# Optimization experiments

Hardware: AMD Instinct MI355X
Metric: run time of the kernel (lower is better)

## Reference

```python
import jax, jax.numpy as jnp
import numpy as np

N = 16384
E = 65536

def _nnconv(x, src, dst, edge_attr, A, b, root, bias, c_in, c_out):
    # edge MLP: [E,2] -> [E, c_in*c_out], ReLU
    W = jax.nn.relu(edge_attr @ A + b).reshape(E, c_in, c_out)
    # gather source features, per-edge matmul: [E,c_in] x [E,c_in,c_out] -> [E,c_out]
    msg = jnp.einsum('ei,eio->eo', x[src], W)
    # scatter-add to target nodes
    agg = jax.ops.segment_sum(msg, dst, num_segments=N)
    return agg + x @ root + bias

def setup_inputs() -> dict:
    key = jax.random.key(0)
    ks = jax.random.split(key, 12)
    inp = {
        'x': jax.random.normal(ks[0], (N, 8), dtype=jnp.float32),
        'edge_index': jax.random.randint(ks[1], (2, E), 0, N, dtype=jnp.int64),
        'edge_attr': jax.random.normal(ks[2], (E, 2), dtype=jnp.float32),
        # edge-MLP 1: Linear(2, 512)
        'A1': jax.random.normal(ks[3], (2, 512), dtype=jnp.float32) * (1.0 / np.sqrt(2.0)),
        'b1': jnp.zeros((512,), dtype=jnp.float32),
        # edge-MLP 2: Linear(2, 4096)
        'A2': jax.random.normal(ks[4], (2, 4096), dtype=jnp.float32) * (1.0 / np.sqrt(2.0)),
        'b2': jnp.zeros((4096,), dtype=jnp.float32),
        # NNConv root weights + biases
        'root1': jax.random.normal(ks[5], (8, 64), dtype=jnp.float32) * (1.0 / np.sqrt(8.0)),
        'bias1': jnp.zeros((64,), dtype=jnp.float32),
        'root2': jax.random.normal(ks[6], (64, 64), dtype=jnp.float32) * (1.0 / np.sqrt(64.0)),
        'bias2': jnp.zeros((64,), dtype=jnp.float32),
    }
    return inp

def reference(x, edge_index, edge_attr, A1, b1, A2, b2, root1, bias1, root2, bias2):
    src = edge_index[0]  # x_j (message source)
    dst = edge_index[1]  # aggregation target
    h = _nnconv(x, src, dst, edge_attr, A1, b1, root1, bias1, 8, 64)
    h = _nnconv(h, src, dst, edge_attr, A2, b2, root2, bias2, 64, 64)
    return h
```

## Files before the change

kernel.cpp:

```cpp
#include <hip/hip_runtime.h>

#define N_NODES 16384
#define N_EDGES 65536

typedef float f32x16 __attribute__((ext_vector_type(16)));
typedef float f32x8  __attribute__((ext_vector_type(8)));
typedef float f32x4  __attribute__((ext_vector_type(4)));

__device__ __forceinline__ float rfl_f(float v) {
    int i = __builtin_amdgcn_readfirstlane(__builtin_bit_cast(int, v));
    return __builtin_bit_cast(float, i);
}

__global__ void k_node1(const float* __restrict__ x, const float* __restrict__ root1,
                        const float* __restrict__ bias1, float* __restrict__ h1) {
    int t = blockIdx.x * blockDim.x + threadIdx.x;
    int n = t >> 6, o = t & 63;
    float acc = bias1[o];
#pragma unroll
    for (int i = 0; i < 8; ++i)
        acc = fmaf(x[n * 8 + i], root1[i * 64 + o], acc);
    h1[t] = acc;
}

__global__ __launch_bounds__(256)
void k_edge1(const float* __restrict__ x, const int* __restrict__ ei,
             const float* __restrict__ ea, const float* __restrict__ A1,
             const float* __restrict__ b1, float* __restrict__ h1) {
    int lane = threadIdx.x & 63;
    f32x8 W0, W1, BB;
#pragma unroll
    for (int i = 0; i < 8; ++i) {
        W0[i] = A1[i * 64 + lane];
        W1[i] = A1[512 + i * 64 + lane];
        BB[i] = b1[i * 64 + lane];
    }
    asm volatile("" : "+v"(W0), "+v"(W1), "+v"(BB));

    int wid = blockIdx.x * (blockDim.x >> 6) + (threadIdx.x >> 6);
    int nw = gridDim.x * (blockDim.x >> 6);
#pragma clang loop unroll(disable)
    for (int p = wid; p < N_EDGES / 2; p += nw) {
        int2 srcp = ((const int2*)ei)[p];
        int2 dstp = ((const int2*)(ei + N_EDGES))[p];
        float4 eap = ((const float4*)ea)[p];
        int s0 = __builtin_amdgcn_readfirstlane(srcp.x);
        int s1 = __builtin_amdgcn_readfirstlane(srcp.y);
        int d0 = __builtin_amdgcn_readfirstlane(dstp.x);
        int d1 = __builtin_amdgcn_readfirstlane(dstp.y);
        float ea00 = rfl_f(eap.x), ea01 = rfl_f(eap.y);
        float ea10 = rfl_f(eap.z), ea11 = rfl_f(eap.w);
        const float* xp0 = x + (size_t)s0 * 8;
        const float* xp1 = x + (size_t)s1 * 8;
        f32x8 ha, hb;
        asm volatile("s_load_dwordx8 %0, %2, 0x0\n\t"
                     "s_load_dwordx8 %1, %3, 0x0\n\t"
                     "s_waitcnt lgkmcnt(0)"
                     : "=&s"(ha), "=&s"(hb) : "s"(xp0), "s"(xp1));
        float acc0 = 0.f, acc1 = 0.f;
#pragma unroll
        for (int i = 0; i < 8; ++i) {
            float wva = fmaxf(fmaf(ea01, W1[i], fmaf(ea00, W0[i], BB[i])), 0.f);
            acc0 = fmaf(ha[i], wva, acc0);
            float wvb = fmaxf(fmaf(ea11, W1[i], fmaf(ea10, W0[i], BB[i])), 0.f);
            acc1 = fmaf(hb[i], wvb, acc1);
        }
        atomicAdd(&h1[(size_t)d0 * 64 + lane], acc0);
        atomicAdd(&h1[(size_t)d1 * 64 + lane], acc1);
    }
}

__global__ __launch_bounds__(256)
void k_node2(const float* __restrict__ h1, const float* __restrict__ root2,
             const float* __restrict__ bias2, float* __restrict__ out) {
    int lane = threadIdx.x & 63;
    f32x16 R0, R1, R2, R3;
#pragma unroll
    for (int i = 0; i < 16; ++i) {
        R0[i] = root2[(i)      * 64 + lane];
        R1[i] = root2[(16 + i) * 64 + lane];
        R2[i] = root2[(32 + i) * 64 + lane];
        R3[i] = root2[(48 + i) * 64 + lane];
    }
    asm volatile("" : "+v"(R0), "+v"(R1), "+v"(R2), "+v"(R3));
    float bias = bias2[lane];

    int wid = blockIdx.x * (blockDim.x >> 6) + (threadIdx.x >> 6);
    int nw = gridDim.x * (blockDim.x >> 6);
#pragma clang loop unroll(disable)
    for (int n = wid; n < N_NODES; n += nw) {
        int nu = __builtin_amdgcn_readfirstlane(n);
        const float* hp = h1 + (size_t)nu * 64;
        f32x16 h0, h1v, h2, h3;
        asm volatile("s_load_dwordx16 %0, %4, 0x0\n\t"
                     "s_load_dwordx16 %1, %4, 0x40\n\t"
                     "s_load_dwordx16 %2, %4, 0x80\n\t"
                     "s_load_dwordx16 %3, %4, 0xc0\n\t"
                     "s_waitcnt lgkmcnt(0)"
                     : "=&s"(h0), "=&s"(h1v), "=&s"(h2), "=&s"(h3) : "s"(hp));
        float acc = bias;
#pragma unroll
        for (int i = 0; i < 16; ++i) acc = fmaf(h0[i],  R0[i], acc);
#pragma unroll
        for (int i = 0; i < 16; ++i) acc = fmaf(h1v[i], R1[i], acc);
#pragma unroll
        for (int i = 0; i < 16; ++i) acc = fmaf(h2[i],  R2[i], acc);
#pragma unroll
        for (int i = 0; i < 16; ++i) acc = fmaf(h3[i],  R3[i], acc);
        out[(size_t)nu * 64 + lane] = acc;
    }
}

__global__ __launch_bounds__(256)
void k_edge2(const float* __restrict__ h1, const int* __restrict__ ei,
             const float* __restrict__ ea, const float* __restrict__ A2,
             const float* __restrict__ b2, float* __restrict__ out) {
    __shared__ __align__(16) float WT[3 * 64 * 36];
    int half = blockIdx.x & 1;
    for (int j = threadIdx.x; j < 2048; j += 256) {
        int i = j >> 6, o = j & 63;
        WT[o * 36 + i]                = A2[half * 2048 + j];
        WT[64 * 36 + o * 36 + i]      = A2[4096 + half * 2048 + j];
        WT[2 * 64 * 36 + o * 36 + i]  = b2[half * 2048 + j];
    }
    __syncthreads();

    int lane = threadIdx.x & 63;
    int base = half * 32;
    unsigned laddr = (unsigned)(uintptr_t)WT + lane * 144;

    int g = blockIdx.x >> 1;
    int wslot = g * 4 + (threadIdx.x >> 6);
#pragma clang loop unroll(disable)
    for (int p = wslot; p < N_EDGES / 2; p += 4096) {
        int2 srcp = ((const int2*)ei)[p];
        int2 dstp = ((const int2*)(ei + N_EDGES))[p];
        float4 eap = ((const float4*)ea)[p];
        int s0 = __builtin_amdgcn_readfirstlane(srcp.x);
        int s1 = __builtin_amdgcn_readfirstlane(srcp.y);
        int d0 = __builtin_amdgcn_readfirstlane(dstp.x);
        int d1 = __builtin_amdgcn_readfirstlane(dstp.y);
        float ea00 = rfl_f(eap.x), ea01 = rfl_f(eap.y);
        float ea10 = rfl_f(eap.z), ea11 = rfl_f(eap.w);
        const float* hp0 = h1 + (size_t)s0 * 64 + base;
        const float* hp1 = h1 + (size_t)s1 * 64 + base;

        f32x16 ha, hb, hc, hd;
        asm volatile("s_load_dwordx16 %0, %4, 0x0\n\t"
                     "s_load_dwordx16 %1, %4, 0x40\n\t"
                     "s_load_dwordx16 %2, %5, 0x0\n\t"
                     "s_load_dwordx16 %3, %5, 0x40"
                     : "=&s"(ha), "=&s"(hb), "=&s"(hc), "=&s"(hd)
                     : "s"(hp0), "s"(hp1));

        f32x4 wa[8], wb[8], wc[8];
        asm volatile(
            "ds_read_b128 %0, %12 offset:0\n\t"
            "ds_read_b128 %1, %12 offset:16\n\t"
            "ds_read_b128 %2, %12 offset:32\n\t"
            "ds_read_b128 %3, %12 offset:48\n\t"
            "ds_read_b128 %4, %12 offset:9216\n\t"
            "ds_read_b128 %5, %12 offset:9232\n\t"
            "ds_read_b128 %6, %12 offset:9248\n\t"
            "ds_read_b128 %7, %12 offset:9264\n\t"
            "ds_read_b128 %8, %12 offset:18432\n\t"
            "ds_read_b128 %9, %12 offset:18448\n\t"
            "ds_read_b128 %10, %12 offset:18464\n\t"
            "ds_read_b128 %11, %12 offset:18480"
            : "=&v"(wa[0]), "=&v"(wa[1]), "=&v"(wa[2]), "=&v"(wa[3]),
              "=&v"(wb[0]), "=&v"(wb[1]), "=&v"(wb[2]), "=&v"(wb[3]),
              "=&v"(wc[0]), "=&v"(wc[1]), "=&v"(wc[2]), "=&v"(wc[3])
            : "v"(laddr));
        asm volatile(
            "ds_read_b128 %0, %12 offset:64\n\t"
            "ds_read_b128 %1, %12 offset:80\n\t"
            "ds_read_b128 %2, %12 offset:96\n\t"
            "ds_read_b128 %3, %12 offset:112\n\t"
            "ds_read_b128 %4, %12 offset:9280\n\t"
            "ds_read_b128 %5, %12 offset:9296\n\t"
            "ds_read_b128 %6, %12 offset:9312\n\t"
            "ds_read_b128 %7, %12 offset:9328\n\t"
            "ds_read_b128 %8, %12 offset:18496\n\t"
            "ds_read_b128 %9, %12 offset:18512\n\t"
            "ds_read_b128 %10, %12 offset:18528\n\t"
            "ds_read_b128 %11, %12 offset:18544"
            : "=&v"(wa[4]), "=&v"(wa[5]), "=&v"(wa[6]), "=&v"(wa[7]),
              "=&v"(wb[4]), "=&v"(wb[5]), "=&v"(wb[6]), "=&v"(wb[7]),
              "=&v"(wc[4]), "=&v"(wc[5]), "=&v"(wc[6]), "=&v"(wc[7])
            : "v"(laddr));
        asm volatile("s_waitcnt lgkmcnt(0)"
            : "+v"(wa[0]), "+v"(wa[1]), "+v"(wa[2]), "+v"(wa[3]),
              "+v"(wa[4]), "+v"(wa[5]), "+v"(wa[6]), "+v"(wa[7]),
              "+v"(wb[0]), "+v"(wb[1]), "+v"(wb[2]), "+v"(wb[3]),
              "+v"(wb[4]), "+v"(wb[5]), "+v"(wb[6]), "+v"(wb[7]),
              "+v"(wc[0]), "+v"(wc[1]), "+v"(wc[2]), "+v"(wc[3]),
              "+v"(wc[4]), "+v"(wc[5]), "+v"(wc[6]), "+v"(wc[7]),
              "+s"(ha), "+s"(hb), "+s"(hc), "+s"(hd));

        float acc0 = 0.f, acc1 = 0.f;
#pragma unroll
        for (int q = 0; q < 4; ++q) {
#pragma unroll
            for (int k = 0; k < 4; ++k) {
                float wv0 = fmaxf(fmaf(ea01, wb[q][k], fmaf(ea00, wa[q][k], wc[q][k])), 0.f);
                acc0 = fmaf(ha[q * 4 + k], wv0, acc0);
                float wv1 = fmaxf(fmaf(ea11, wb[q][k], fmaf(ea10, wa[q][k], wc[q][k])), 0.f);
                acc1 = fmaf(hc[q * 4 + k], wv1, acc1);
            }
        }
#pragma unroll
        for (int q = 4; q < 8; ++q) {
#pragma unroll
            for (int k = 0; k < 4; ++k) {
                float wv0 = fmaxf(fmaf(ea01, wb[q][k], fmaf(ea00, wa[q][k], wc[q][k])), 0.f);
                acc0 = fmaf(hb[(q - 4) * 4 + k], wv0, acc0);
                float wv1 = fmaxf(fmaf(ea11, wb[q][k], fmaf(ea10, wa[q][k], wc[q][k])), 0.f);
                acc1 = fmaf(hd[(q - 4) * 4 + k], wv1, acc1);
            }
        }
        atomicAdd(&out[(size_t)d0 * 64 + lane], acc0);
        atomicAdd(&out[(size_t)d1 * 64 + lane], acc1);
    }
}

extern "C" void kernel_launch(void* const* d_in, const int* in_sizes, int n_in,
                              void* d_out, int out_size, void* d_ws, size_t ws_size,
                              hipStream_t stream) {
    const float* x     = (const float*)d_in[0];
    const int*   ei    = (const int*)d_in[1];
    const float* ea    = (const float*)d_in[2];
    const float* A1    = (const float*)d_in[3];
    const float* b1    = (const float*)d_in[4];
    const float* A2    = (const float*)d_in[5];
    const float* b2    = (const float*)d_in[6];
    const float* root1 = (const float*)d_in[7];
    const float* bias1 = (const float*)d_in[8];
    const float* root2 = (const float*)d_in[9];
    const float* bias2 = (const float*)d_in[10];
    float* out = (float*)d_out;
    float* h1  = (float*)d_ws;

    k_node1<<<N_NODES * 64 / 256, 256, 0, stream>>>(x, root1, bias1, h1);
    k_edge1<<<2048, 256, 0, stream>>>(x, ei, ea, A1, b1, h1);
    k_node2<<<1024, 256, 0, stream>>>(h1, root2, bias2, out);
    k_edge2<<<2048, 256, 0, stream>>>(h1, ei, ea, A2, b2, out);
}
```

Baseline: 144.3 us.

## Software-pipeline edge2 loop by prefetching next source rows and edge data

Restructures the layer-2 edge loop so that the scalar loads of the next iteration's source-node feature rows are issued partway through the current iteration's FMA work. Edge indices and attributes are fetched two iterations ahead. This aims to hide the latency of the dependent scalar-memory gather behind compute. The risk is that the inline-asm s_load results are written asynchronously into SGPRs the compiler believes are already defined, and that pressure on scalar and vector registers goes up.

```diff
diff --git a/kernel.cpp b/kernel.cpp
--- a/kernel.cpp
+++ b/kernel.cpp
@@ -119,40 +119,44 @@
     int half = blockIdx.x & 1;
     for (int j = threadIdx.x; j < 2048; j += 256) {
         int i = j >> 6, o = j & 63;
-        WT[o * 36 + i]                = A2[half * 2048 + j];
-        WT[64 * 36 + o * 36 + i]      = A2[4096 + half * 2048 + j];
-        WT[2 * 64 * 36 + o * 36 + i]  = b2[half * 2048 + j];
+        WT[o * 36 + i]               = A2[half * 2048 + j];
+        WT[64 * 36 + o * 36 + i]     = A2[4096 + half * 2048 + j];
+        WT[2 * 64 * 36 + o * 36 + i] = b2[half * 2048 + j];
     }
     __syncthreads();
 
     int lane = threadIdx.x & 63;
-    int base = half * 32;
+    int base = __builtin_amdgcn_readfirstlane(half * 32);
     unsigned laddr = (unsigned)(uintptr_t)WT + lane * 144;
 
     int g = blockIdx.x >> 1;
     int wslot = g * 4 + (threadIdx.x >> 6);
-#pragma clang loop unroll(disable)
-    for (int p = wslot; p < N_EDGES / 2; p += 4096) {
-        int2 srcp = ((const int2*)ei)[p];
-        int2 dstp = ((const int2*)(ei + N_EDGES))[p];
-        float4 eap = ((const float4*)ea)[p];
-        int s0 = __builtin_amdgcn_readfirstlane(srcp.x);
-        int s1 = __builtin_amdgcn_readfirstlane(srcp.y);
-        int d0 = __builtin_amdgcn_readfirstlane(dstp.x);
-        int d1 = __builtin_amdgcn_readfirstlane(dstp.y);
-        float ea00 = rfl_f(eap.x), ea01 = rfl_f(eap.y);
-        float ea10 = rfl_f(eap.z), ea11 = rfl_f(eap.w);
+
+    f32x16 ha, hb, hc, hd;
+
+    int p0 = wslot;
+    int2   dst_c = ((const int2*)(ei + N_EDGES))[p0];
+    float4 ea_c  = ((const float4*)ea)[p0];
+    {
+        int2 src0 = ((const int2*)ei)[p0];
+        int s0 = __builtin_amdgcn_readfirstlane(src0.x);
+        int s1 = __builtin_amdgcn_readfirstlane(src0.y);
         const float* hp0 = h1 + (size_t)s0 * 64 + base;
         const float* hp1 = h1 + (size_t)s1 * 64 + base;
-
-        f32x16 ha, hb, hc, hd;
         asm volatile("s_load_dwordx16 %0, %4, 0x0\n\t"
                      "s_load_dwordx16 %1, %4, 0x40\n\t"
                      "s_load_dwordx16 %2, %5, 0x0\n\t"
                      "s_load_dwordx16 %3, %5, 0x40"
                      : "=&s"(ha), "=&s"(hb), "=&s"(hc), "=&s"(hd)
                      : "s"(hp0), "s"(hp1));
-
+    }
+    int pn = p0 + 4096; if (pn > N_EDGES / 2 - 1) pn = N_EDGES / 2 - 1;
+    int2   src_n = ((const int2*)ei)[pn];
+    int2   dst_n = ((const int2*)(ei + N_EDGES))[pn];
+    float4 ea_n  = ((const float4*)ea)[pn];
+
+#pragma clang loop unroll(disable)
+    for (int p = wslot; p < N_EDGES / 2; p += 4096) {
         f32x4 wa[8], wb[8], wc[8];
         asm volatile(
             "ds_read_b128 %0, %12 offset:0\n\t"
@@ -188,6 +192,12 @@
               "=&v"(wb[4]), "=&v"(wb[5]), "=&v"(wb[6]), "=&v"(wb[7]),
               "=&v"(wc[4]), "=&v"(wc[5]), "=&v"(wc[6]), "=&v"(wc[7])
             : "v"(laddr));
+
+        int s0n = __builtin_amdgcn_readfirstlane(src_n.x);
+        int s1n = __builtin_amdgcn_readfirstlane(src_n.y);
+        const float* hpn0 = h1 + (size_t)s0n * 64 + base;
+        const float* hpn1 = h1 + (size_t)s1n * 64 + base;
+
         asm volatile("s_waitcnt lgkmcnt(0)"
             : "+v"(wa[0]), "+v"(wa[1]), "+v"(wa[2]), "+v"(wa[3]),
               "+v"(wa[4]), "+v"(wa[5]), "+v"(wa[6]), "+v"(wa[7]),
@@ -202,24 +212,37 @@
         for (int q = 0; q < 4; ++q) {
 #pragma unroll
             for (int k = 0; k < 4; ++k) {
-                float wv0 = fmaxf(fmaf(ea01, wb[q][k], fmaf(ea00, wa[q][k], wc[q][k])), 0.f);
+                float wv0 = fmaxf(fmaf(ea_c.y, wb[q][k], fmaf(ea_c.x, wa[q][k], wc[q][k])), 0.f);
                 acc0 = fmaf(ha[q * 4 + k], wv0, acc0);
-                float wv1 = fmaxf(fmaf(ea11, wb[q][k], fmaf(ea10, wa[q][k], wc[q][k])), 0.f);
+                float wv1 = fmaxf(fmaf(ea_c.w, wb[q][k], fmaf(ea_c.z, wa[q][k], wc[q][k])), 0.f);
                 acc1 = fmaf(hc[q * 4 + k], wv1, acc1);
             }
         }
+        asm volatile("s_load_dwordx16 %0, %2, 0x0\n\t"
+                     "s_load_dwordx16 %1, %3, 0x0"
+                     : "=&s"(ha), "=&s"(hc) : "s"(hpn0), "s"(hpn1));
 #pragma unroll
         for (int q = 4; q < 8; ++q) {
 #pragma unroll
             for (int k = 0; k < 4; ++k) {
-                float wv0 = fmaxf(fmaf(ea01, wb[q][k], fmaf(ea00, wa[q][k], wc[q][k])), 0.f);
+                float wv0 = fmaxf(fmaf(ea_c.y, wb[q][k], fmaf(ea_c.x, wa[q][k], wc[q][k])), 0.f);
                 acc0 = fmaf(hb[(q - 4) * 4 + k], wv0, acc0);
-                float wv1 = fmaxf(fmaf(ea11, wb[q][k], fmaf(ea10, wa[q][k], wc[q][k])), 0.f);
+                float wv1 = fmaxf(fmaf(ea_c.w, wb[q][k], fmaf(ea_c.z, wa[q][k], wc[q][k])), 0.f);
                 acc1 = fmaf(hd[(q - 4) * 4 + k], wv1, acc1);
             }
         }
-        atomicAdd(&out[(size_t)d0 * 64 + lane], acc0);
-        atomicAdd(&out[(size_t)d1 * 64 + lane], acc1);
+        asm volatile("s_load_dwordx16 %0, %2, 0x40\n\t"
+                     "s_load_dwordx16 %1, %3, 0x40"
+                     : "=&s"(hb), "=&s"(hd) : "s"(hpn0), "s"(hpn1));
+
+        atomicAdd(&out[(size_t)dst_c.x * 64 + lane], acc0);
+        atomicAdd(&out[(size_t)dst_c.y * 64 + lane], acc1);
+
+        dst_c = dst_n; ea_c = ea_n;
+        int pn2 = p + 8192; if (pn2 > N_EDGES / 2 - 1) pn2 = N_EDGES / 2 - 1;
+        src_n = ((const int2*)ei)[pn2];
+        dst_n = ((const int2*)(ei + N_EDGES))[pn2];
+        ea_n  = ((const float4*)ea)[pn2];
     }
 }
 
```

Result: faster. 138.5 us (-4.0%).
